# Kernel optimization log

Measured on AMD Instinct MI355X. Metric: run time of the kernel, lower is better.

## Reference

```python
import jax, jax.numpy as jnp
import numpy as np

C_EM, H_EM, C_A = 256, 8, 32
S, R = 1024, 256
LN_EPS = 1e-5
MASK_BIAS = 1e9


def setup_inputs() -> dict:
    key = jax.random.key(0)
    ks = jax.random.split(key, 8)
    sc = 0.02
    m = jax.random.normal(ks[0], (S, R, C_EM), jnp.float32)
    # binary column mask (float mask in the original; int here so it is a constant)
    mask = (jax.random.uniform(ks[1], (S, R)) < 0.9).astype(jnp.int32)
    return {
        "m": m,
        "ln_g": jnp.ones((C_EM,), jnp.float32),
        "ln_b": jnp.zeros((C_EM,), jnp.float32),
        "w_q": jax.random.normal(ks[2], (C_EM, H_EM, C_A), jnp.float32) * sc,
        "w_k": jax.random.normal(ks[3], (C_EM, C_A), jnp.float32) * sc,
        "w_v": jax.random.normal(ks[4], (C_EM, C_A), jnp.float32) * sc,
        "w_g": jax.random.normal(ks[5], (C_EM, H_EM, C_A), jnp.float32) * sc,
        "b_g": jnp.zeros((H_EM, C_A), jnp.float32),
        "w_o": jax.random.normal(ks[6], (H_EM, C_A, C_EM), jnp.float32) * sc,
        "b_o": jnp.zeros((C_EM,), jnp.float32),
        "mask": mask,
    }


def reference(m, ln_g, ln_b, w_q, w_k, w_v, w_g, b_g, w_o, b_o, mask):
    maskf = mask.astype(m.dtype)  # [s, r]
    # LayerNorm over c_em (biased variance, eps=1e-5, torch default)
    mu = jnp.mean(m, axis=-1, keepdims=True)
    var = jnp.mean((m - mu) ** 2, axis=-1, keepdims=True)
    x = (m - mu) * jax.lax.rsqrt(var + LN_EPS) * ln_g + ln_b  # [s, r, c]
    # masked mean-pool over s -> per-column query
    q_pool = jnp.sum(x * maskf[..., None], axis=-3) / (jnp.sum(maskf, axis=-2)[..., None] + 1e-10)  # [r, c]
    Q = jnp.einsum('rc,chd->rhd', q_pool, w_q) * (1.0 / np.sqrt(C_A))  # [r, h, d]
    K = jnp.einsum('src,cd->srd', x, w_k)  # [s, r, d]
    V = jnp.einsum('src,cd->srd', x, w_v)  # [s, r, d]
    G = jax.nn.sigmoid(jnp.einsum('src,chd->srhd', x, w_g) + b_g)  # [s, r, h, d]
    bias = (maskf - 1.0) * MASK_BIAS  # [s, r]
    logits = jnp.einsum('rhd,srd->srh', Q, K) + bias[..., None]  # [s, r, h]
    A = jax.nn.softmax(logits, axis=-3)  # softmax over s
    O = jnp.einsum('srh,srd->rhd', A, V)  # [r, h, d]
    out = jnp.einsum('srhd,hdc->src', O[None, :, :, :] * G, w_o) + b_o  # [s, r, c]
    return out
```

## Files before the change

kernel.cpp:

```cpp
#include <hip/hip_runtime.h>
#include <math.h>

#define S_DIM 1024
#define R_DIM 256
#define C_DIM 256
#define SCALE 0.17677669529663687f

typedef short bf16x8 __attribute__((ext_vector_type(8)));
typedef float f32x4 __attribute__((ext_vector_type(4)));

__device__ __forceinline__ float wred(float v) {
#pragma unroll
  for (int m = 32; m >= 1; m >>= 1) v += __shfl_xor(v, m, 64);
  return v;
}

__device__ __forceinline__ short f2bf(float f) {
  union { float f; unsigned u; } v;
  v.f = f;
  unsigned r = v.u + 0x7fffu + ((v.u >> 16) & 1u);
  return (short)(r >> 16);
}

__device__ __forceinline__ float bf2f(short s) {
  union { unsigned u; float f; } v;
  v.u = ((unsigned)(unsigned short)s) << 16;
  return v.f;
}

__global__ __launch_bounds__(256)
void k0_prep(const float* __restrict__ w_g, const float* __restrict__ w_o,
             const float* __restrict__ w_k, const float* __restrict__ w_v,
             short* __restrict__ wgB, short* __restrict__ woB,
             short* __restrict__ wkvB) {
  const int id = blockIdx.x * 256 + threadIdx.x;
  if (id < 16384) {
    const int which = id >> 13;
    const int s = id & 8191;
    const int n = s & 255, g = (s >> 8) & 3, kb = s >> 10;
    const float* W = which ? w_o : w_g;
    short* Out = which ? woB : wgB;
#pragma unroll
    for (int j = 0; j < 8; ++j)
      Out[(((size_t)kb * 256 + n) * 4 + g) * 8 + j] =
          f2bf(W[(size_t)(kb * 32 + g * 8 + j) * 256 + n]);
  } else {
    const int s = id - 16384;
    const int n = s & 63, g = (s >> 6) & 3, kb = s >> 8;
    const float* W = (n < 32) ? w_k : w_v;
    const int nn = n & 31;
#pragma unroll
    for (int j = 0; j < 8; ++j)
      wkvB[(((size_t)kb * 64 + n) * 4 + g) * 8 + j] =
          f2bf(W[(size_t)(kb * 32 + g * 8 + j) * 32 + nn]);
  }
}

__global__ __launch_bounds__(256, 3)
void k1_ln_kv(const float* __restrict__ mIn, const float* __restrict__ ln_g,
              const float* __restrict__ ln_b, const short* __restrict__ wkvB,
              const int* __restrict__ mask,
              float* __restrict__ K_ws, float* __restrict__ V_ws,
              float* __restrict__ pool_ws, char* xout) {
  __shared__ __align__(16) short A_lds[2048 * 8];
  __shared__ float mask_s[64];
  __shared__ float4 poolp[4][64];
  const int r  = blockIdx.y;
  const int s0 = blockIdx.x * 64;
  const int t  = threadIdx.x;

  if (t < 64) mask_s[t] = mask[(s0 + t) * R_DIM + r] ? 1.f : 0.f;

  {
    const int rw = t >> 2;
    const int q  = t & 3;
    const size_t p = (size_t)(s0 + rw) * R_DIM + r;
    const float* src = mIn + p * C_DIM + q * 64;
    float4 xv[16];
    float sum = 0.f, ssq = 0.f;
#pragma unroll
    for (int i = 0; i < 16; ++i) {
      xv[i] = *(const float4*)(src + i * 4);
      sum += xv[i].x + xv[i].y + xv[i].z + xv[i].w;
      ssq += xv[i].x * xv[i].x + xv[i].y * xv[i].y + xv[i].z * xv[i].z +
             xv[i].w * xv[i].w;
    }
    sum += __shfl_xor(sum, 1, 64); ssq += __shfl_xor(ssq, 1, 64);
    sum += __shfl_xor(sum, 2, 64); ssq += __shfl_xor(ssq, 2, 64);
    const float mu = sum * (1.f / 256.f);
    const float var = ssq * (1.f / 256.f) - mu * mu;
    const float rs = rsqrtf(var + 1e-5f);

    const int gw = rw >> 4;
    const int lf0 = rw & 15;
#pragma unroll
    for (int kh = 0; kh < 2; ++kh) {
      const int kb = 2 * q + kh;
#pragma unroll
      for (int g = 0; g < 4; ++g) {
        const int lidx = kh * 32 + g * 8;
        const float4 a0 = xv[lidx >> 2], a1 = xv[(lidx >> 2) + 1];
        const float4 g0 = *(const float4*)(ln_g + kb * 32 + g * 8);
        const float4 g1 = *(const float4*)(ln_g + kb * 32 + g * 8 + 4);
        const float4 b0 = *(const float4*)(ln_b + kb * 32 + g * 8);
        const float4 b1 = *(const float4*)(ln_b + kb * 32 + g * 8 + 4);
        bf16x8 f;
        f[0] = f2bf((a0.x - mu) * rs * g0.x + b0.x);
        f[1] = f2bf((a0.y - mu) * rs * g0.y + b0.y);
        f[2] = f2bf((a0.z - mu) * rs * g0.z + b0.z);
        f[3] = f2bf((a0.w - mu) * rs * g0.w + b0.w);
        f[4] = f2bf((a1.x - mu) * rs * g1.x + b1.x);
        f[5] = f2bf((a1.y - mu) * rs * g1.y + b1.y);
        f[6] = f2bf((a1.z - mu) * rs * g1.z + b1.z);
        f[7] = f2bf((a1.w - mu) * rs * g1.w + b1.w);
        int byte = (((gw * 8 + kb) * 64 + lf0 + g * 16) << 4) ^ (((kb >> 1) & 3) << 5);
        *(bf16x8*)((char*)A_lds + byte) = f;
      }
    }
  }
  __syncthreads();

  {
#pragma unroll
    for (int i = 0; i < 8; ++i) {
      const int u = i * 256 + t;
      const bf16x8 v = *(const bf16x8*)((const char*)A_lds + u * 16);
      *(bf16x8*)(xout + ((size_t)((s0 + (u >> 5)) * R_DIM + r)) * 1024 +
                 (u & 31) * 16) = v;
    }
  }

  {
    const int w = t >> 6, l = t & 63;
    const int lm = l & 15, g = l >> 4;
    f32x4 acc[4];
#pragma unroll
    for (int ni = 0; ni < 4; ++ni) acc[ni] = (f32x4){0.f, 0.f, 0.f, 0.f};
#pragma unroll
    for (int kb = 0; kb < 8; ++kb) {
      const int byte = (((w * 8 + kb) * 64 + l) << 4) ^ (((kb >> 1) & 3) << 5);
      const bf16x8 a = *(const bf16x8*)((char*)A_lds + byte);
      bf16x8 bfr[4];
#pragma unroll
      for (int ni = 0; ni < 4; ++ni)
        bfr[ni] = *(const bf16x8*)(wkvB + (((size_t)kb * 64 + lm + ni * 16) * 4 + g) * 8);
#pragma unroll
      for (int ni = 0; ni < 4; ++ni)
        acc[ni] = __builtin_amdgcn_mfma_f32_16x16x32_bf16(a, bfr[ni], acc[ni], 0, 0, 0);
    }
#pragma unroll
    for (int ni = 0; ni < 4; ++ni) {
      const int col = lm + ni * 16;
      float* Out = (col < 32) ? K_ws : V_ws;
      const int cc = col & 31;
#pragma unroll
      for (int reg = 0; reg < 4; ++reg) {
        const int s = s0 + w * 16 + g * 4 + reg;
        Out[((size_t)s * R_DIM + r) * 32 + cc] = acc[ni][reg];
      }
    }
  }

  {
    const int lc = t & 63;
    const int wq = t >> 6;
    const int kb = lc >> 3, g2 = (lc >> 1) & 3, bh = (lc & 1) * 4;
    float4 ps = make_float4(0.f, 0.f, 0.f, 0.f);
    for (int i = 0; i < 16; ++i) {
      const int rloc = (i + lc) & 15;
      const int byte =
          ((((wq * 8 + kb) * 64 + rloc + g2 * 16) << 4) + bh * 2) ^ (((kb >> 1) & 3) << 5);
      const short4 xb = *(const short4*)((char*)A_lds + byte);
      const float mk = mask_s[wq * 16 + rloc];
      ps.x += mk * bf2f(xb.x);
      ps.y += mk * bf2f(xb.y);
      ps.z += mk * bf2f(xb.z);
      ps.w += mk * bf2f(xb.w);
    }
    poolp[wq][lc] = ps;
  }
  __syncthreads();
  if (t < 64) {
    const float4 a = poolp[0][t], b = poolp[1][t], c = poolp[2][t], d = poolp[3][t];
    atomicAdd(&pool_ws[r * C_DIM + t * 4 + 0], a.x + b.x + c.x + d.x);
    atomicAdd(&pool_ws[r * C_DIM + t * 4 + 1], a.y + b.y + c.y + d.y);
    atomicAdd(&pool_ws[r * C_DIM + t * 4 + 2], a.z + b.z + c.z + d.z);
    atomicAdd(&pool_ws[r * C_DIM + t * 4 + 3], a.w + b.w + c.w + d.w);
  }
}

__global__ __launch_bounds__(256, 2)
void k2_q(const float* __restrict__ pool_ws, const int* __restrict__ mask,
          const float* __restrict__ w_q, float* __restrict__ Q_ws) {
  __shared__ float qp[256];
  __shared__ float wsum[4];
  const int r = blockIdx.x, t = threadIdx.x;
  int cnt = 0;
  for (int s = t; s < S_DIM; s += 256) cnt += mask[s * R_DIM + r];
  float cf = wred((float)cnt);
  if ((t & 63) == 0) wsum[t >> 6] = cf;
  __syncthreads();
  const float denom = wsum[0] + wsum[1] + wsum[2] + wsum[3] + 1e-10f;
  qp[t] = pool_ws[r * C_DIM + t] / denom;
  __syncthreads();
  float acc = 0.f;
  for (int c = 0; c < 256; ++c) acc += qp[c] * w_q[c * 256 + t];
  Q_ws[r * 256 + t] = acc * SCALE;
}

__global__ __launch_bounds__(256, 2)
void k3_attn(const float* __restrict__ K_ws, const float* __restrict__ V_ws,
             const int* __restrict__ mask, const float* __restrict__ Q_ws,
             float* __restrict__ O_ws) {
  __shared__ float q[256];
  __shared__ float lg[1024 * 9];
  __shared__ float kv[256 * 36];
  __shared__ float mh[8], inv[8];
  const int r = blockIdx.x, t = threadIdx.x;
  q[t] = Q_ws[r * 256 + t];

  for (int ch = 0; ch < 4; ++ch) {
    const int sb = ch * 256;
    __syncthreads();
    for (int f = t; f < 2048; f += 256) {
      const int sl = f >> 3, dq = f & 7;
      *(float4*)(kv + sl * 36 + dq * 4) =
          *(const float4*)(K_ws + ((size_t)(sb + sl) * R_DIM + r) * 32 + dq * 4);
    }
    __syncthreads();
    float kr[32];
#pragma unroll
    for (int dq = 0; dq < 8; ++dq)
      *(float4*)(kr + dq * 4) = *(float4*)(kv + t * 36 + dq * 4);
    const float bias = mask[(sb + t) * R_DIM + r] ? 0.f : -1e9f;
#pragma unroll
    for (int h = 0; h < 8; ++h) {
      float a = 0.f;
#pragma unroll
      for (int d = 0; d < 32; ++d) a += q[h * 32 + d] * kr[d];
      lg[(sb + t) * 9 + h] = a + bias;
    }
  }
  __syncthreads();
  {
    const int h = t >> 5, l32 = t & 31;
    float mx = -INFINITY;
    for (int k = 0; k < 32; ++k) mx = fmaxf(mx, lg[(l32 + 32 * k) * 9 + h]);
#pragma unroll
    for (int mk = 16; mk >= 1; mk >>= 1) mx = fmaxf(mx, __shfl_xor(mx, mk, 64));
    float sm = 0.f;
    for (int k = 0; k < 32; ++k) sm += expf(lg[(l32 + 32 * k) * 9 + h] - mx);
#pragma unroll
    for (int mk = 16; mk >= 1; mk >>= 1) sm += __shfl_xor(sm, mk, 64);
    if (l32 == 0) { mh[h] = mx; inv[h] = 1.f / sm; }
  }
  __syncthreads();
  for (int f = t; f < 8192; f += 256) {
    const int s = f >> 3, h = f & 7;
    lg[s * 9 + h] = expf(lg[s * 9 + h] - mh[h]) * inv[h];
  }
  const int h = t >> 5, d = t & 31;
  float o = 0.f;
  for (int ch = 0; ch < 4; ++ch) {
    const int sb = ch * 256;
    __syncthreads();
    for (int f = t; f < 2048; f += 256) {
      const int sl = f >> 3, dq = f & 7;
      *(float4*)(kv + sl * 36 + dq * 4) =
          *(const float4*)(V_ws + ((size_t)(sb + sl) * R_DIM + r) * 32 + dq * 4);
    }
    __syncthreads();
    for (int sl = 0; sl < 256; ++sl)
      o += lg[(sb + sl) * 9 + h] * kv[sl * 36 + d];
  }
  O_ws[r * 256 + t] = o;
}

__global__ __launch_bounds__(256, 3)
void k4_mfma(const short* __restrict__ wgB, const float* __restrict__ b_g,
             const float* __restrict__ O_ws, const short* __restrict__ woB,
             const float* __restrict__ b_o, float* outx) {
  __shared__ __align__(16) short T_lds[2048 * 8];
  const int t = threadIdx.x;
  const int s0 = blockIdx.x * 64;
  const int r  = blockIdx.y;
  const int l = t & 63, w = t >> 6, lm = l & 15, g = l >> 4;
  const char* outB = (const char*)outx;
  const int col = w * 64 + lm;

  float o4[4], bg4[4], bo4[4];
#pragma unroll
  for (int ni = 0; ni < 4; ++ni) {
    o4[ni] = O_ws[r * 256 + col + ni * 16];
    bg4[ni] = b_g[col + ni * 16];
    bo4[ni] = b_o[col + ni * 16];
  }

  f32x4 acc[4][4];
#pragma unroll
  for (int ni = 0; ni < 4; ++ni)
#pragma unroll
    for (int mi = 0; mi < 4; ++mi)
      acc[mi][ni] = (f32x4){bg4[ni], bg4[ni], bg4[ni], bg4[ni]};

#pragma unroll
  for (int kb = 0; kb < 8; ++kb) {
    const int cc = ((kb >> 1) & 3) << 1;
    bf16x8 a[4], bb[4];
#pragma unroll
    for (int mi = 0; mi < 4; ++mi) {
      const int u = ((mi * 8 + kb) * 64 + l) ^ cc;
      a[mi] = *(const bf16x8*)(outB +
              ((size_t)((s0 + (u >> 5)) * R_DIM + r)) * 1024 + (u & 31) * 16);
    }
#pragma unroll
    for (int ni = 0; ni < 4; ++ni)
      bb[ni] = *(const bf16x8*)(wgB + (((size_t)kb * 256 + col + ni * 16) * 4 + g) * 8);
#pragma unroll
    for (int mi = 0; mi < 4; ++mi)
#pragma unroll
      for (int ni = 0; ni < 4; ++ni)
        acc[mi][ni] = __builtin_amdgcn_mfma_f32_16x16x32_bf16(a[mi], bb[ni], acc[mi][ni], 0, 0, 0);
  }

#pragma unroll
  for (int mi = 0; mi < 4; ++mi)
#pragma unroll
    for (int ni = 0; ni < 4; ++ni) {
      const int c2 = col + ni * 16;
      const int kb2 = c2 >> 5, g2 = (c2 >> 3) & 3, b2 = c2 & 7;
#pragma unroll
      for (int reg = 0; reg < 4; ++reg) {
        const float tv = o4[ni] / (1.f + __expf(-acc[mi][ni][reg]));
        T_lds[((mi * 8 + kb2) * 64 + (g * 4 + reg) + g2 * 16) * 8 + b2] = f2bf(tv);
      }
    }
  __syncthreads();

#pragma unroll
  for (int ni = 0; ni < 4; ++ni)
#pragma unroll
    for (int mi = 0; mi < 4; ++mi)
      acc[mi][ni] = (f32x4){bo4[ni], bo4[ni], bo4[ni], bo4[ni]};
#pragma unroll
  for (int kb = 0; kb < 8; ++kb) {
    bf16x8 a[4], bb[4];
#pragma unroll
    for (int mi = 0; mi < 4; ++mi)
      a[mi] = *(const bf16x8*)(T_lds + ((mi * 8 + kb) * 64 + l) * 8);
#pragma unroll
    for (int ni = 0; ni < 4; ++ni)
      bb[ni] = *(const bf16x8*)(woB + (((size_t)kb * 256 + col + ni * 16) * 4 + g) * 8);
#pragma unroll
    for (int mi = 0; mi < 4; ++mi)
#pragma unroll
      for (int ni = 0; ni < 4; ++ni)
        acc[mi][ni] = __builtin_amdgcn_mfma_f32_16x16x32_bf16(a[mi], bb[ni], acc[mi][ni], 0, 0, 0);
  }

#pragma unroll
  for (int mi = 0; mi < 4; ++mi)
#pragma unroll
    for (int ni = 0; ni < 4; ++ni)
#pragma unroll
      for (int reg = 0; reg < 4; ++reg) {
        const int row = mi * 16 + g * 4 + reg;
        outx[((size_t)((s0 + row) * R_DIM + r)) * 256 + col + ni * 16] =
            acc[mi][ni][reg];
      }
}

extern "C" void kernel_launch(void* const* d_in, const int* in_sizes, int n_in,
                              void* d_out, int out_size, void* d_ws, size_t ws_size,
                              hipStream_t stream) {
  const float* mIn  = (const float*)d_in[0];
  const float* ln_g = (const float*)d_in[1];
  const float* ln_b = (const float*)d_in[2];
  const float* w_q  = (const float*)d_in[3];
  const float* w_k  = (const float*)d_in[4];
  const float* w_v  = (const float*)d_in[5];
  const float* w_g  = (const float*)d_in[6];
  const float* b_g  = (const float*)d_in[7];
  const float* w_o  = (const float*)d_in[8];
  const float* b_o  = (const float*)d_in[9];
  const int*   mask = (const int*)d_in[10];
  float* outp = (float*)d_out;

  char* ws = (char*)d_ws;
  const size_t NP = (size_t)S_DIM * R_DIM;
  float* K_ws    = (float*)ws;
  float* V_ws    = K_ws + NP * 32;
  float* pool_ws = V_ws + NP * 32;
  float* Q_ws    = pool_ws + 65536;
  float* O_ws    = Q_ws + 65536;
  short* wgB     = (short*)(O_ws + 65536);
  short* woB     = wgB + 65536;
  short* wkvB    = woB + 65536;

  hipMemsetAsync(pool_ws, 0, 65536 * sizeof(float), stream);

  k0_prep<<<72, 256, 0, stream>>>(w_g, w_o, w_k, w_v, wgB, woB, wkvB);
  k1_ln_kv<<<dim3(S_DIM / 64, R_DIM), 256, 0, stream>>>(
      mIn, ln_g, ln_b, wkvB, mask, K_ws, V_ws, pool_ws, (char*)outp);
  k2_q<<<R_DIM, 256, 0, stream>>>(pool_ws, mask, w_q, Q_ws);
  k3_attn<<<R_DIM, 256, 0, stream>>>(K_ws, V_ws, mask, Q_ws, O_ws);
  k4_mfma<<<dim3(S_DIM / 64, R_DIM), 256, 0, stream>>>(
      wgB, b_g, O_ws, woB, b_o, outp);
}
```

Baseline: 398.0 us.

## Move gate projection into LN kernel and store gate logits instead of normalized x

The gate GEMM (x·w_g + b_g) now runs in k1 while the normalized x tile is still in LDS. k1 writes the bf16 gate pre-activations to the output buffer as scratch instead of x itself. k4 then only reads those logits, applies sigmoid times O when forming the A fragments, and runs the single w_o GEMM. This removes one GEMM pass and the LDS round trip from k4, and raises its occupancy hint. The cost is much higher register pressure in k1 (16 extra f32x4 accumulators) and more sigmoid work per element in k4.

```diff
diff --git a/kernel.cpp b/kernel.cpp
--- a/kernel.cpp
+++ b/kernel.cpp
@@ -59,9 +59,10 @@
 __global__ __launch_bounds__(256, 3)
 void k1_ln_kv(const float* __restrict__ mIn, const float* __restrict__ ln_g,
               const float* __restrict__ ln_b, const short* __restrict__ wkvB,
+              const short* __restrict__ wgB, const float* __restrict__ b_g,
               const int* __restrict__ mask,
               float* __restrict__ K_ws, float* __restrict__ V_ws,
-              float* __restrict__ pool_ws, char* xout) {
+              float* __restrict__ pool_ws, char* glout) {
   __shared__ __align__(16) short A_lds[2048 * 8];
   __shared__ float mask_s[64];
   __shared__ float4 poolp[4][64];
@@ -120,33 +121,35 @@
   }
   __syncthreads();
 
+  const int w = t >> 6, l = t & 63;
+  const int lm = l & 15, g = l >> 4;
+
+  f32x4 gacc[16];
   {
-#pragma unroll
-    for (int i = 0; i < 8; ++i) {
-      const int u = i * 256 + t;
-      const bf16x8 v = *(const bf16x8*)((const char*)A_lds + u * 16);
-      *(bf16x8*)(xout + ((size_t)((s0 + (u >> 5)) * R_DIM + r)) * 1024 +
-                 (u & 31) * 16) = v;
-    }
-  }
-
-  {
-    const int w = t >> 6, l = t & 63;
-    const int lm = l & 15, g = l >> 4;
     f32x4 acc[4];
 #pragma unroll
     for (int ni = 0; ni < 4; ++ni) acc[ni] = (f32x4){0.f, 0.f, 0.f, 0.f};
+#pragma unroll
+    for (int ni = 0; ni < 16; ++ni) {
+      const float bg = b_g[lm + ni * 16];
+      gacc[ni] = (f32x4){bg, bg, bg, bg};
+    }
 #pragma unroll
     for (int kb = 0; kb < 8; ++kb) {
       const int byte = (((w * 8 + kb) * 64 + l) << 4) ^ (((kb >> 1) & 3) << 5);
       const bf16x8 a = *(const bf16x8*)((char*)A_lds + byte);
-      bf16x8 bfr[4];
-#pragma unroll
-      for (int ni = 0; ni < 4; ++ni)
-        bfr[ni] = *(const bf16x8*)(wkvB + (((size_t)kb * 64 + lm + ni * 16) * 4 + g) * 8);
-#pragma unroll
-      for (int ni = 0; ni < 4; ++ni)
-        acc[ni] = __builtin_amdgcn_mfma_f32_16x16x32_bf16(a, bfr[ni], acc[ni], 0, 0, 0);
+#pragma unroll
+      for (int ni = 0; ni < 4; ++ni) {
+        const bf16x8 bkv =
+            *(const bf16x8*)(wkvB + (((size_t)kb * 64 + lm + ni * 16) * 4 + g) * 8);
+        acc[ni] = __builtin_amdgcn_mfma_f32_16x16x32_bf16(a, bkv, acc[ni], 0, 0, 0);
+      }
+#pragma unroll
+      for (int ni = 0; ni < 16; ++ni) {
+        const bf16x8 bg8 =
+            *(const bf16x8*)(wgB + (((size_t)kb * 256 + lm + ni * 16) * 4 + g) * 8);
+        gacc[ni] = __builtin_amdgcn_mfma_f32_16x16x32_bf16(a, bg8, gacc[ni], 0, 0, 0);
+      }
     }
 #pragma unroll
     for (int ni = 0; ni < 4; ++ni) {
@@ -180,12 +183,36 @@
     poolp[wq][lc] = ps;
   }
   __syncthreads();
+
+#pragma unroll
+  for (int ni = 0; ni < 16; ++ni) {
+    const int cb = 2 * ni + (lm >> 3);
+    const int kb2 = cb >> 2, c4 = cb & 3, j = lm & 7;
+#pragma unroll
+    for (int reg = 0; reg < 4; ++reg) {
+      const int byte =
+          ((((w * 8 + kb2) * 64 + c4 * 16 + g * 4 + reg) << 4) + j * 2) ^
+          (((kb2 >> 1) & 3) << 5);
+      *(short*)((char*)A_lds + byte) = f2bf(gacc[ni][reg]);
+    }
+  }
   if (t < 64) {
     const float4 a = poolp[0][t], b = poolp[1][t], c = poolp[2][t], d = poolp[3][t];
     atomicAdd(&pool_ws[r * C_DIM + t * 4 + 0], a.x + b.x + c.x + d.x);
     atomicAdd(&pool_ws[r * C_DIM + t * 4 + 1], a.y + b.y + c.y + d.y);
     atomicAdd(&pool_ws[r * C_DIM + t * 4 + 2], a.z + b.z + c.z + d.z);
     atomicAdd(&pool_ws[r * C_DIM + t * 4 + 3], a.w + b.w + c.w + d.w);
+  }
+  __syncthreads();
+
+#pragma unroll
+  for (int i = 0; i < 8; ++i) {
+    const int u = i * 256 + t;
+    const int kbu = (u >> 6) & 7;
+    const int byte = (u << 4) ^ (((kbu >> 1) & 3) << 5);
+    const bf16x8 v = *(const bf16x8*)((const char*)A_lds + byte);
+    *(bf16x8*)(glout + ((size_t)((s0 + (u >> 5)) * R_DIM + r)) * 1024 +
+               (u & 31) * 16) = v;
   }
 }
 
@@ -276,46 +303,50 @@
   O_ws[r * 256 + t] = o;
 }
 
-__global__ __launch_bounds__(256, 3)
-void k4_mfma(const short* __restrict__ wgB, const float* __restrict__ b_g,
-             const float* __restrict__ O_ws, const short* __restrict__ woB,
+__global__ __launch_bounds__(256, 4)
+void k4_mfma(const float* __restrict__ O_ws, const short* __restrict__ woB,
              const float* __restrict__ b_o, float* outx) {
-  __shared__ __align__(16) short T_lds[2048 * 8];
   const int t = threadIdx.x;
   const int s0 = blockIdx.x * 64;
   const int r  = blockIdx.y;
   const int l = t & 63, w = t >> 6, lm = l & 15, g = l >> 4;
-  const char* outB = (const char*)outx;
+  const char* glB = (const char*)outx;
   const int col = w * 64 + lm;
 
-  float o4[4], bg4[4], bo4[4];
+  f32x4 acc[4][4];
 #pragma unroll
   for (int ni = 0; ni < 4; ++ni) {
-    o4[ni] = O_ws[r * 256 + col + ni * 16];
-    bg4[ni] = b_g[col + ni * 16];
-    bo4[ni] = b_o[col + ni * 16];
-  }
-
-  f32x4 acc[4][4];
-#pragma unroll
-  for (int ni = 0; ni < 4; ++ni)
+    const float bo = b_o[col + ni * 16];
 #pragma unroll
     for (int mi = 0; mi < 4; ++mi)
-      acc[mi][ni] = (f32x4){bg4[ni], bg4[ni], bg4[ni], bg4[ni]};
+      acc[mi][ni] = (f32x4){bo, bo, bo, bo};
+  }
 
 #pragma unroll
   for (int kb = 0; kb < 8; ++kb) {
-    const int cc = ((kb >> 1) & 3) << 1;
-    bf16x8 a[4], bb[4];
+    const float4 o0 = *(const float4*)(O_ws + r * 256 + kb * 32 + g * 8);
+    const float4 o1 = *(const float4*)(O_ws + r * 256 + kb * 32 + g * 8 + 4);
+    bf16x8 a[4];
 #pragma unroll
     for (int mi = 0; mi < 4; ++mi) {
-      const int u = ((mi * 8 + kb) * 64 + l) ^ cc;
-      a[mi] = *(const bf16x8*)(outB +
-              ((size_t)((s0 + (u >> 5)) * R_DIM + r)) * 1024 + (u & 31) * 16);
-    }
+      const int u = (mi * 8 + kb) * 64 + l;
+      const bf16x8 raw = *(const bf16x8*)(glB +
+          ((size_t)((s0 + (u >> 5)) * R_DIM + r)) * 1024 + (u & 31) * 16);
+      bf16x8 af;
+      af[0] = f2bf(o0.x / (1.f + __expf(-bf2f(raw[0]))));
+      af[1] = f2bf(o0.y / (1.f + __expf(-bf2f(raw[1]))));
+      af[2] = f2bf(o0.z / (1.f + __expf(-bf2f(raw[2]))));
+      af[3] = f2bf(o0.w / (1.f + __expf(-bf2f(raw[3]))));
+      af[4] = f2bf(o1.x / (1.f + __expf(-bf2f(raw[4]))));
+      af[5] = f2bf(o1.y / (1.f + __expf(-bf2f(raw[5]))));
+      af[6] = f2bf(o1.z / (1.f + __expf(-bf2f(raw[6]))));
+      af[7] = f2bf(o1.w / (1.f + __expf(-bf2f(raw[7]))));
+      a[mi] = af;
+    }
+    bf16x8 bb[4];
 #pragma unroll
     for (int ni = 0; ni < 4; ++ni)
-      bb[ni] = *(const bf16x8*)(wgB + (((size_t)kb * 256 + col + ni * 16) * 4 + g) * 8);
+      bb[ni] = *(const bf16x8*)(woB + (((size_t)kb * 256 + col + ni * 16) * 4 + g) * 8);
 #pragma unroll
     for (int mi = 0; mi < 4; ++mi)
 #pragma unroll
@@ -323,40 +354,7 @@
         acc[mi][ni] = __builtin_amdgcn_mfma_f32_16x16x32_bf16(a[mi], bb[ni], acc[mi][ni], 0, 0, 0);
   }
 
-#pragma unroll
-  for (int mi = 0; mi < 4; ++mi)
-#pragma unroll
-    for (int ni = 0; ni < 4; ++ni) {
-      const int c2 = col + ni * 16;
-      const int kb2 = c2 >> 5, g2 = (c2 >> 3) & 3, b2 = c2 & 7;
-#pragma unroll
-      for (int reg = 0; reg < 4; ++reg) {
-        const float tv = o4[ni] / (1.f + __expf(-acc[mi][ni][reg]));
-        T_lds[((mi * 8 + kb2) * 64 + (g * 4 + reg) + g2 * 16) * 8 + b2] = f2bf(tv);
-      }
-    }
-  __syncthreads();
-
-#pragma unroll
-  for (int ni = 0; ni < 4; ++ni)
-#pragma unroll
-    for (int mi = 0; mi < 4; ++mi)
-      acc[mi][ni] = (f32x4){bo4[ni], bo4[ni], bo4[ni], bo4[ni]};
-#pragma unroll
-  for (int kb = 0; kb < 8; ++kb) {
-    bf16x8 a[4], bb[4];
-#pragma unroll
-    for (int mi = 0; mi < 4; ++mi)
-      a[mi] = *(const bf16x8*)(T_lds + ((mi * 8 + kb) * 64 + l) * 8);
-#pragma unroll
-    for (int ni = 0; ni < 4; ++ni)
-      bb[ni] = *(const bf16x8*)(woB + (((size_t)kb * 256 + col + ni * 16) * 4 + g) * 8);
-#pragma unroll
-    for (int mi = 0; mi < 4; ++mi)
-#pragma unroll
-      for (int ni = 0; ni < 4; ++ni)
-        acc[mi][ni] = __builtin_amdgcn_mfma_f32_16x16x32_bf16(a[mi], bb[ni], acc[mi][ni], 0, 0, 0);
-  }
+  __syncthreads();
 
 #pragma unroll
   for (int mi = 0; mi < 4; ++mi)
@@ -401,9 +399,9 @@
 
   k0_prep<<<72, 256, 0, stream>>>(w_g, w_o, w_k, w_v, wgB, woB, wkvB);
   k1_ln_kv<<<dim3(S_DIM / 64, R_DIM), 256, 0, stream>>>(
-      mIn, ln_g, ln_b, wkvB, mask, K_ws, V_ws, pool_ws, (char*)outp);
+      mIn, ln_g, ln_b, wkvB, wgB, b_g, mask, K_ws, V_ws, pool_ws, (char*)outp);
   k2_q<<<R_DIM, 256, 0, stream>>>(pool_ws, mask, w_q, Q_ws);
   k3_attn<<<R_DIM, 256, 0, stream>>>(K_ws, V_ws, mask, Q_ws, O_ws);
   k4_mfma<<<dim3(S_DIM / 64, R_DIM), 256, 0, stream>>>(
-      wgB, b_g, O_ws, woB, b_o, outp);
-}
+      O_ws, woB, b_o, outp);
+}
```

New measurement: 544.0 us. 36.7% more time.

## Stage normalized activations through LDS in output kernel and swizzle gate tile

Applied to the files above, without the earlier changes.

The output kernel now loads the bf16 normalized-activation tile for its block from global memory into shared memory with coalesced vector loads, then feeds the gate MFMA from LDS instead of doing scattered per-lane global loads. The same LDS buffer is reused for the gated tile, with an XOR swizzle meant to reduce bank conflicts, and the launch bound asks for 4 blocks per CU. Smaller edits use fast exp and a reciprocal intrinsic for the sigmoid, and move the activation store in k1 after its MFMA. The extra barriers and the register staging could reduce overlap, and fast math slightly lowers precision.

```diff
diff --git a/kernel.cpp b/kernel.cpp
--- a/kernel.cpp
+++ b/kernel.cpp
@@ -26,6 +26,10 @@
   union { unsigned u; float f; } v;
   v.u = ((unsigned)(unsigned short)s) << 16;
   return v.f;
+}
+
+__device__ __forceinline__ float fast_sigmoid_mul(float o, float gl) {
+  return o * __builtin_amdgcn_rcpf(1.f + __expf(-gl));
 }
 
 __global__ __launch_bounds__(256)
@@ -61,7 +65,7 @@
               const float* __restrict__ ln_b, const short* __restrict__ wkvB,
               const int* __restrict__ mask,
               float* __restrict__ K_ws, float* __restrict__ V_ws,
-              float* __restrict__ pool_ws, char* xout) {
+              float* __restrict__ pool_ws, char* __restrict__ xout) {
   __shared__ __align__(16) short A_lds[2048 * 8];
   __shared__ float mask_s[64];
   __shared__ float4 poolp[4][64];
@@ -121,16 +125,6 @@
   __syncthreads();
 
   {
-#pragma unroll
-    for (int i = 0; i < 8; ++i) {
-      const int u = i * 256 + t;
-      const bf16x8 v = *(const bf16x8*)((const char*)A_lds + u * 16);
-      *(bf16x8*)(xout + ((size_t)((s0 + (u >> 5)) * R_DIM + r)) * 1024 +
-                 (u & 31) * 16) = v;
-    }
-  }
-
-  {
     const int w = t >> 6, l = t & 63;
     const int lm = l & 15, g = l >> 4;
     f32x4 acc[4];
@@ -159,6 +153,14 @@
         Out[((size_t)s * R_DIM + r) * 32 + cc] = acc[ni][reg];
       }
     }
+  }
+
+#pragma unroll
+  for (int i = 0; i < 8; ++i) {
+    const int u = i * 256 + t;
+    const bf16x8 v = *(const bf16x8*)((const char*)A_lds + u * 16);
+    *(bf16x8*)(xout + ((size_t)((s0 + (u >> 5)) * R_DIM + r)) * 1024 +
+               (u & 31) * 16) = v;
   }
 
   {
@@ -249,7 +251,7 @@
 #pragma unroll
     for (int mk = 16; mk >= 1; mk >>= 1) mx = fmaxf(mx, __shfl_xor(mx, mk, 64));
     float sm = 0.f;
-    for (int k = 0; k < 32; ++k) sm += expf(lg[(l32 + 32 * k) * 9 + h] - mx);
+    for (int k = 0; k < 32; ++k) sm += __expf(lg[(l32 + 32 * k) * 9 + h] - mx);
 #pragma unroll
     for (int mk = 16; mk >= 1; mk >>= 1) sm += __shfl_xor(sm, mk, 64);
     if (l32 == 0) { mh[h] = mx; inv[h] = 1.f / sm; }
@@ -257,7 +259,7 @@
   __syncthreads();
   for (int f = t; f < 8192; f += 256) {
     const int s = f >> 3, h = f & 7;
-    lg[s * 9 + h] = expf(lg[s * 9 + h] - mh[h]) * inv[h];
+    lg[s * 9 + h] = __expf(lg[s * 9 + h] - mh[h]) * inv[h];
   }
   const int h = t >> 5, d = t & 31;
   float o = 0.f;
@@ -276,22 +278,34 @@
   O_ws[r * 256 + t] = o;
 }
 
-__global__ __launch_bounds__(256, 3)
+__global__ __launch_bounds__(256, 4)
 void k4_mfma(const short* __restrict__ wgB, const float* __restrict__ b_g,
              const float* __restrict__ O_ws, const short* __restrict__ woB,
-             const float* __restrict__ b_o, float* outx) {
-  __shared__ __align__(16) short T_lds[2048 * 8];
+             const float* __restrict__ b_o, float* __restrict__ outx) {
+  __shared__ __align__(16) short A_lds[2048 * 8];
   const int t = threadIdx.x;
   const int s0 = blockIdx.x * 64;
   const int r  = blockIdx.y;
   const int l = t & 63, w = t >> 6, lm = l & 15, g = l >> 4;
-  const char* outB = (const char*)outx;
+  const char* glB = (const char*)outx;
+
+  bf16x8 stg[8];
+#pragma unroll
+  for (int i = 0; i < 8; ++i) {
+    const int u = i * 256 + t;
+    stg[i] = *(const bf16x8*)(glB +
+        ((size_t)((s0 + (u >> 5)) * R_DIM + r)) * 1024 + (u & 31) * 16);
+  }
+#pragma unroll
+  for (int i = 0; i < 8; ++i)
+    *(bf16x8*)((char*)A_lds + (i * 256 + t) * 16) = stg[i];
+  __syncthreads();
+
   const int col = w * 64 + lm;
-
   float o4[4], bg4[4], bo4[4];
 #pragma unroll
   for (int ni = 0; ni < 4; ++ni) {
-    o4[ni] = O_ws[r * 256 + col + ni * 16];
+    o4[ni]  = O_ws[r * 256 + col + ni * 16];
     bg4[ni] = b_g[col + ni * 16];
     bo4[ni] = b_o[col + ni * 16];
   }
@@ -305,14 +319,11 @@
 
 #pragma unroll
   for (int kb = 0; kb < 8; ++kb) {
-    const int cc = ((kb >> 1) & 3) << 1;
+    const int swz = ((kb >> 1) & 3) << 5;
     bf16x8 a[4], bb[4];
 #pragma unroll
-    for (int mi = 0; mi < 4; ++mi) {
-      const int u = ((mi * 8 + kb) * 64 + l) ^ cc;
-      a[mi] = *(const bf16x8*)(outB +
-              ((size_t)((s0 + (u >> 5)) * R_DIM + r)) * 1024 + (u & 31) * 16);
-    }
+    for (int mi = 0; mi < 4; ++mi)
+      a[mi] = *(const bf16x8*)((char*)A_lds + ((((mi * 8 + kb) * 64 + l) << 4) ^ swz));
 #pragma unroll
     for (int ni = 0; ni < 4; ++ni)
       bb[ni] = *(const bf16x8*)(wgB + (((size_t)kb * 256 + col + ni * 16) * 4 + g) * 8);
@@ -322,19 +333,23 @@
       for (int ni = 0; ni < 4; ++ni)
         acc[mi][ni] = __builtin_amdgcn_mfma_f32_16x16x32_bf16(a[mi], bb[ni], acc[mi][ni], 0, 0, 0);
   }
-
-#pragma unroll
-  for (int mi = 0; mi < 4; ++mi)
+  __syncthreads();
+
+#pragma unroll
+  for (int mi = 0; mi < 4; ++mi) {
 #pragma unroll
     for (int ni = 0; ni < 4; ++ni) {
       const int c2 = col + ni * 16;
       const int kb2 = c2 >> 5, g2 = (c2 >> 3) & 3, b2 = c2 & 7;
 #pragma unroll
       for (int reg = 0; reg < 4; ++reg) {
-        const float tv = o4[ni] / (1.f + __expf(-acc[mi][ni][reg]));
-        T_lds[((mi * 8 + kb2) * 64 + (g * 4 + reg) + g2 * 16) * 8 + b2] = f2bf(tv);
+        const float tv = fast_sigmoid_mul(o4[ni], acc[mi][ni][reg]);
+        const int u = (mi * 8 + kb2) * 64 + (g * 4 + reg) + g2 * 16;
+        const int byte = ((u << 4) ^ (((u >> 4) & 3) << 4)) + b2 * 2;
+        *(short*)((char*)A_lds + byte) = f2bf(tv);
       }
     }
+  }
   __syncthreads();
 
 #pragma unroll
@@ -346,8 +361,10 @@
   for (int kb = 0; kb < 8; ++kb) {
     bf16x8 a[4], bb[4];
 #pragma unroll
-    for (int mi = 0; mi < 4; ++mi)
-      a[mi] = *(const bf16x8*)(T_lds + ((mi * 8 + kb) * 64 + l) * 8);
+    for (int mi = 0; mi < 4; ++mi) {
+      const int u = (mi * 8 + kb) * 64 + l;
+      a[mi] = *(const bf16x8*)((char*)A_lds + ((u << 4) ^ (g << 4)));
+    }
 #pragma unroll
     for (int ni = 0; ni < 4; ++ni)
       bb[ni] = *(const bf16x8*)(woB + (((size_t)kb * 256 + col + ni * 16) * 4 + g) * 8);
```

Result: no change. 393.6 us (-1.1%).
